# Optimization experiments

Measured on AMD Instinct MI355X. Metric: run time of the kernel, lower is better.

The kernel has to match this reference:

```python
import jax, jax.numpy as jnp
import numpy as np

N_EMBD = 1024
N_HEAD = 16
B, L = 4, 2048


def setup_inputs() -> dict:
    key = jax.random.key(0)
    ks = jax.random.split(key, 5)
    scale = 1.0 / np.sqrt(N_EMBD)
    x = jax.random.normal(ks[0], (B, L, N_EMBD), dtype=jnp.float32)
    # nn.Linear(n_embd, n_embd, bias=False) weights, stored torch-style (out, in)
    Wq = jax.random.uniform(ks[1], (N_EMBD, N_EMBD), jnp.float32, -scale, scale)
    Wk = jax.random.uniform(ks[2], (N_EMBD, N_EMBD), jnp.float32, -scale, scale)
    Wv = jax.random.uniform(ks[3], (N_EMBD, N_EMBD), jnp.float32, -scale, scale)
    Wp = jax.random.uniform(ks[4], (N_EMBD, N_EMBD), jnp.float32, -scale, scale)
    attn_mask = jnp.ones((B, L), dtype=jnp.int32)
    return {"x": x, "Wq": Wq, "Wk": Wk, "Wv": Wv, "Wp": Wp, "attn_mask": attn_mask}


def reference(x, Wq, Wk, Wv, Wp, attn_mask):
    Bq, Lq, C = x.shape
    hd = C // N_HEAD
    # torch Linear: y = x @ W.T
    def split_heads(y):
        return y.reshape(Bq, Lq, N_HEAD, hd).transpose(0, 2, 1, 3)  # (B,H,L,hd)
    q = split_heads(x @ Wq.T)
    k = split_heads(x @ Wk.T)
    v = split_heads(x @ Wv.T)
    att = jnp.einsum("bhqd,bhkd->bhqk", q, k) / np.sqrt(hd)  # (B,H,L,L)
    causal = jnp.tril(jnp.ones((Lq, Lq), dtype=bool))
    neg_inf = jnp.float32(-jnp.inf)
    att = jnp.where(causal[None, None, :, :], att, neg_inf)
    pad = (attn_mask != 0)[:, None, None, :]  # (B,1,1,L) key-side padding mask
    att = jnp.where(pad, att, neg_inf)
    att = jax.nn.softmax(att, axis=-1)
    y = jnp.einsum("bhqk,bhkd->bhqd", att, v)
    y = y.transpose(0, 2, 1, 3).reshape(Bq, Lq, C)
    return y @ Wp.T
```

## Files before the change

### kernel.cpp

```cpp
#include <hip/hip_runtime.h>

typedef __attribute__((ext_vector_type(8))) short short8;
typedef __attribute__((ext_vector_type(4))) float floatx4;

#define CEMB 1024
#define NHEAD 16
#define HD 64
#define BATCH 4
#define SEQ 2048

#define BARRIER() asm volatile("s_waitcnt lgkmcnt(0)\n\ts_barrier" ::: "memory")

__device__ __forceinline__ unsigned short f2bf(float f) {
    union { float f; unsigned int i; } x; x.f = f;
    unsigned int r = x.i + 0x7FFFu + ((x.i >> 16) & 1u);
    return (unsigned short)(r >> 16);
}
__device__ __forceinline__ unsigned int packbf_trunc(float a, float b) {
    union { float f; unsigned int u; } x, y; x.f = a; y.f = b;
    return (x.u >> 16) | (y.u & 0xFFFF0000u);
}

#define GLD16(gp, lp) \
    __builtin_amdgcn_global_load_lds((const __attribute__((address_space(1))) void*)(gp), \
                                     (__attribute__((address_space(3))) void*)(lp), 16, 0, 0)

__global__ void cast_x(const float* __restrict__ src, unsigned short* __restrict__ dst, int n4) {
    int i = blockIdx.x * blockDim.x + threadIdx.x;
    if (i < n4) {
        float4 v = ((const float4*)src)[i];
        ushort4 o;
        o.x = f2bf(v.x); o.y = f2bf(v.y); o.z = f2bf(v.z); o.w = f2bf(v.w);
        ((ushort4*)dst)[i] = o;
    }
}

__global__ void cast_w(const float* __restrict__ w0, const float* __restrict__ w1,
                       const float* __restrict__ w2, const float* __restrict__ w3,
                       unsigned short* __restrict__ o0, unsigned short* __restrict__ o1,
                       unsigned short* __restrict__ o2, unsigned short* __restrict__ o3) {
    int which = blockIdx.y;
    const float* src = which == 0 ? w0 : which == 1 ? w1 : which == 2 ? w2 : w3;
    unsigned short* dst = which == 0 ? o0 : which == 1 ? o1 : which == 2 ? o2 : o3;
    float scale = (which == 0) ? 0.125f * 1.44269504088896f : 1.0f;
    int i = blockIdx.x * blockDim.x + threadIdx.x;
    float4 v = ((const float4*)src)[i];
    ushort4 o;
    o.x = f2bf(v.x * scale); o.y = f2bf(v.y * scale);
    o.z = f2bf(v.z * scale); o.w = f2bf(v.w * scale);
    ((ushort4*)dst)[i] = o;
}


#define MFMA __builtin_amdgcn_mfma_f32_16x16x32_bf16

#define PH(Ab, Bb) do {                                                         \
    short8 af[4][2], bfr[2][2];                                                 \
    _Pragma("unroll")                                                           \
    for (int mm = 0; mm < 4; ++mm) {                                            \
        af[mm][0] = *(const short8*)((Ab) + aOffR + mm*1024 + ck0);             \
        af[mm][1] = *(const short8*)((Ab) + aOffR + mm*1024 + ck1);             \
    }                                                                           \
    _Pragma("unroll")                                                           \
    for (int nn = 0; nn < 2; ++nn) {                                            \
        bfr[nn][0] = *(const short8*)((Bb) + bOffR + nn*1024 + ck0);            \
        bfr[nn][1] = *(const short8*)((Bb) + bOffR + nn*1024 + ck1);            \
    }                                                                           \
    __builtin_amdgcn_s_setprio(1);                                              \
    _Pragma("unroll")                                                           \
    for (int mm = 0; mm < 4; ++mm)                                              \
        _Pragma("unroll")                                                       \
        for (int nn = 0; nn < 2; ++nn) {                                        \
            acc[mm][nn] = MFMA(af[mm][0], bfr[nn][0], acc[mm][nn], 0,0,0);      \
            acc[mm][nn] = MFMA(af[mm][1], bfr[nn][1], acc[mm][nn], 0,0,0);      \
        }                                                                       \
    __builtin_amdgcn_s_setprio(0);                                              \
    __builtin_amdgcn_sched_barrier(0);                                          \
} while (0)

#define STAGE(Ab, Bb, k0) do {                                                  \
    GLD16(aS + (k0),             (Ab) + aLS);                                   \
    GLD16(aS + (k0) +  8 * CEMB, (Ab) + aLS + 512);                             \
    GLD16(aS + (k0) + 16 * CEMB, (Ab) + aLS + 1024);                            \
    GLD16(aS + (k0) + 24 * CEMB, (Ab) + aLS + 1536);                            \
    GLD16(bS + (k0),             (Bb) + aLS);                                   \
    GLD16(bS + (k0) +  8 * CEMB, (Bb) + aLS + 512);                             \
    GLD16(bS + (k0) + 16 * CEMB, (Bb) + aLS + 1024);                            \
    GLD16(bS + (k0) + 24 * CEMB, (Bb) + aLS + 1536);                            \
} while (0)

#define PH4(Ab, Bb, t, do_stage) do {                                           \
    short8 af[4][2], bfr[2][2];                                                 \
    _Pragma("unroll")                                                           \
    for (int mm = 0; mm < 4; ++mm) {                                            \
        af[mm][0] = *(const short8*)((Ab) + aOffR + mm*1024 + ck0);             \
        af[mm][1] = *(const short8*)((Ab) + aOffR + mm*1024 + ck1);             \
    }                                                                           \
    _Pragma("unroll")                                                           \
    for (int nn = 0; nn < 2; ++nn) {                                            \
        bfr[nn][0] = *(const short8*)((Bb) + bOffR + (2+nn)*1024 + ck0);        \
        bfr[nn][1] = *(const short8*)((Bb) + bOffR + (2+nn)*1024 + ck1);        \
    }                                                                           \
    asm volatile("s_waitcnt lgkmcnt(0)\n\ts_barrier" ::: "memory");             \
    __builtin_amdgcn_sched_barrier(0);                                          \
    if (do_stage) STAGE(Ab, Bb, ((t) + 2) * 64);                                \
    __builtin_amdgcn_s_setprio(1);                                              \
    _Pragma("unroll")                                                           \
    for (int mm = 0; mm < 4; ++mm)                                              \
        _Pragma("unroll")                                                       \
        for (int nn = 0; nn < 2; ++nn) {                                        \
            acc[mm][2+nn] = MFMA(af[mm][0], bfr[nn][0], acc[mm][2+nn], 0,0,0);  \
            acc[mm][2+nn] = MFMA(af[mm][1], bfr[nn][1], acc[mm][2+nn], 0,0,0);  \
        }                                                                       \
    __builtin_amdgcn_s_setprio(0);                                              \
    __builtin_amdgcn_sched_barrier(0);                                          \
} while (0)

#define TILE(t, drain, do_stage) do {                                           \
    unsigned short* Ab = &As[(t) & 1][0];                                       \
    unsigned short* Bb = &Bs[(t) & 1][0];                                       \
    if (drain) { asm volatile("s_waitcnt vmcnt(0)" ::: "memory"); }             \
    else       { asm volatile("s_waitcnt vmcnt(8)" ::: "memory"); }             \
    asm volatile("s_barrier" ::: "memory");                                     \
    PH(Ab, Bb);                                                                 \
    PH4(Ab, Bb, t, do_stage);                                                   \
} while (0)

__launch_bounds__(256, 2)
__global__ void gemm_128(const unsigned short* __restrict__ A,
                         const unsigned short* __restrict__ W,
                         void* __restrict__ O0, void* __restrict__ O1,
                         void* __restrict__ O2, int mode, int ntn) {
    __shared__ unsigned short As[2][8192];
    __shared__ unsigned short Bs[2][8192];

    int nwg = gridDim.x;
    int bid = blockIdx.x;
    int wg = (bid & 7) * (nwg >> 3) + (bid >> 3);
    int cpr = ntn >> 2;
    int c = wg >> 5, r = wg & 31;
    int cm = c / cpr, cn = c - cm * cpr;
    int mt = cm * 8 + (r >> 2);
    int nt = cn * 4 + (r & 3);
    int m0 = mt * 128, n0 = nt * 128;

    int tid = threadIdx.x;
    int wave = tid >> 6, lane = tid & 63;
    int l16 = lane & 15, quad = lane >> 4;
    int wm = wave >> 1, wn = wave & 1;

    int srow = lane >> 3;
    int scol = ((lane & 7) ^ srow) * 8;
    const unsigned short* aS = A + (size_t)(m0 + wave * 32 + srow) * CEMB + scol;
    const unsigned short* bS = W + (size_t)(n0 + wave * 32 + srow) * CEMB + scol;
    int aLS = wave * 2048;

    int aOffR = (wm * 64 + l16) * 64;
    int bOffR = (wn * 64 + l16) * 64;
    int ck0 = (quad ^ (l16 & 7)) * 8;
    int ck1 = ck0 ^ 32;

    floatx4 acc[4][4];
    #pragma unroll
    for (int mm = 0; mm < 4; ++mm)
        #pragma unroll
        for (int nn = 0; nn < 4; ++nn) acc[mm][nn] = (floatx4){0.f, 0.f, 0.f, 0.f};

    STAGE(&As[0][0], &Bs[0][0], 0);
    STAGE(&As[1][0], &Bs[1][0], 64);

    #pragma unroll 2
    for (int t = 0; t < 14; ++t) { TILE(t, false, true); }
    TILE(14, false, false);
    TILE(15, true, false);

    if (mode == 1) {
        float* Of = (float*)O0;
        #pragma unroll
        for (int mf = 0; mf < 4; ++mf)
            #pragma unroll
            for (int j = 0; j < 4; ++j) {
                int m = m0 + wm * 64 + mf * 16 + quad * 4 + j;
                #pragma unroll
                for (int nf = 0; nf < 4; ++nf) {
                    int n = n0 + wn * 64 + nf * 16 + l16;
                    Of[(size_t)m * CEMB + n] = acc[mf][nf][j];
                }
            }
    } else {
        int which = n0 >> 10;
        unsigned short* out = (unsigned short*)(which == 0 ? O0 : which == 1 ? O1 : O2);
        if (which < 2) {
            #pragma unroll
            for (int mf = 0; mf < 4; ++mf)
                #pragma unroll
                for (int j = 0; j < 4; ++j) {
                    int m = m0 + wm * 64 + mf * 16 + quad * 4 + j;
                    int bb = m >> 11, ll = m & (SEQ - 1);
                    #pragma unroll
                    for (int nf = 0; nf < 4; ++nf) {
                        int n = (n0 & (CEMB - 1)) + wn * 64 + nf * 16 + l16;
                        int h = n >> 6, d = n & (HD - 1);
                        out[(size_t)((bb * NHEAD + h) * SEQ + ll) * HD + d] =
                            f2bf(acc[mf][nf][j]);
                    }
                }
        } else {
            #pragma unroll
            for (int mf = 0; mf < 4; ++mf) {
                int m = m0 + wm * 64 + mf * 16 + quad * 4;
                int bb = m >> 11, ll = m & (SEQ - 1);
                #pragma unroll
                for (int nf = 0; nf < 4; ++nf) {
                    int n = (n0 & (CEMB - 1)) + wn * 64 + nf * 16 + l16;
                    int h = n >> 6, d = n & (HD - 1);
                    ushort4 o4;
                    o4.x = f2bf(acc[mf][nf][0]); o4.y = f2bf(acc[mf][nf][1]);
                    o4.z = f2bf(acc[mf][nf][2]); o4.w = f2bf(acc[mf][nf][3]);
                    *(ushort4*)&out[(size_t)((bb * NHEAD + h) * HD + d) * SEQ + ll] = o4;
                }
            }
        }
    }
}

__launch_bounds__(256, 2)
__global__ void attn_mfma(const unsigned short* __restrict__ Qb,
                          const unsigned short* __restrict__ Kb,
                          const unsigned short* __restrict__ Vtg,
                          const int* __restrict__ amask,
                          unsigned short* __restrict__ Yb) {
    __shared__ unsigned short Ks[64 * 64];
    __shared__ unsigned short Vs[64 * 64];
    __shared__ unsigned short Ps[128 * 64];

    int tid = threadIdx.x;
    int wave = tid >> 6;
    int lane = tid & 63;
    int l16 = lane & 15;
    int quad = lane >> 4;
    int l7 = l16 & 7;

    int n = blockIdx.x;
    int rr = n >> 8;
    int i = n & 255;
    int base = i & 15;
    int bh = (i >> 4) + (rr << 4);
    int qt = (rr == 0) ? base
           : (rr == 1) ? 15 - base
           : (rr == 2) ? (base ^ 8)
                       : 15 - (base ^ 8);

    int bidx = bh >> 4;
    int h = bh & (NHEAD - 1);
    size_t hbase = (size_t)bh * SEQ * HD;

    int r0 = tid >> 3, p0 = tid & 7;
    int cl = p0 ^ (r0 & 7);
    unsigned short* kDst0 = Ks + r0 * 64 + p0 * 8;
    unsigned short* kDst1 = kDst0 + 32 * 64;
    unsigned short* vDst0 = Vs + r0 * 64 + p0 * 8;
    unsigned short* vDst1 = vDst0 + 32 * 64;
    const unsigned short* kSrc0 = Kb + hbase + (size_t)r0 * HD + cl * 8;
    const unsigned short* kSrc1 = kSrc0 + (size_t)32 * HD;
    const unsigned short* vSrc0 = Vtg + hbase + (size_t)r0 * SEQ + cl * 8;
    const unsigned short* vSrc1 = vSrc0 + (size_t)32 * SEQ;
    const int* mSrc = amask + bidx * SEQ + quad * 4;

    int q0 = qt * 128;
    int nkt = 2 * qt + 2;

    short8 qf[2][2];
    #pragma unroll
    for (int qsub = 0; qsub < 2; ++qsub)
        #pragma unroll
        for (int kk = 0; kk < 2; ++kk)
            qf[qsub][kk] = *(const short8*)(Qb + hbase +
                (size_t)(q0 + wave * 32 + qsub * 16 + l16) * HD + kk * 32 + quad * 8);

    short8 kr0 = *(const short8*)(kSrc0);
    short8 kr1 = *(const short8*)(kSrc1);
    short8 vr0 = *(const short8*)(vSrc0);
    short8 vr1 = *(const short8*)(vSrc1);
    int4 cmi[4];
    #pragma unroll
    for (int t = 0; t < 4; ++t) cmi[t] = *(const int4*)(mSrc + t * 16);

    floatx4 o[2][4];
    #pragma unroll
    for (int qsub = 0; qsub < 2; ++qsub)
        #pragma unroll
        for (int t = 0; t < 4; ++t) o[qsub][t] = (floatx4){0.f, 0.f, 0.f, 0.f};
    float ls[2] = {0.f, 0.f};

    int qw = q0 + wave * 32;

    for (int jt = 0; jt < nkt; ++jt) {
        BARRIER();
        *(short8*)kDst0 = kr0;
        *(short8*)kDst1 = kr1;
        *(short8*)vDst0 = vr0;
        *(short8*)vDst1 = vr1;
        int4 cm[4];
        #pragma unroll
        for (int t = 0; t < 4; ++t) cm[t] = cmi[t];
        if (jt + 1 < nkt) {
            size_t ko = (size_t)(jt + 1) * 64;
            kr0 = *(const short8*)(kSrc0 + ko * HD);
            kr1 = *(const short8*)(kSrc1 + ko * HD);
            vr0 = *(const short8*)(vSrc0 + ko);
            vr1 = *(const short8*)(vSrc1 + ko);
            #pragma unroll
            for (int t = 0; t < 4; ++t) cmi[t] = *(const int4*)(mSrc + (jt + 1) * 64 + t * 16);
        }
        BARRIER();

        if (jt * 64 <= qw + 31) {
            floatx4 sc[2][4];
            #pragma unroll
            for (int qsub = 0; qsub < 2; ++qsub)
                #pragma unroll
                for (int t = 0; t < 4; ++t) sc[qsub][t] = (floatx4){0.f, 0.f, 0.f, 0.f};
            #pragma unroll
            for (int kk = 0; kk < 2; ++kk)
                #pragma unroll
                for (int t = 0; t < 4; ++t) {
                    short8 aK = *(const short8*)(Ks + (t * 16 + l16) * 64 +
                                                 ((kk * 4 + quad) ^ l7) * 8);
                    #pragma unroll
                    for (int qsub = 0; qsub < 2; ++qsub)
                        sc[qsub][t] = __builtin_amdgcn_mfma_f32_16x16x32_bf16(
                            aK, qf[qsub][kk], sc[qsub][t], 0, 0, 0);
                }

            bool needc = (jt * 64 + 63 > qw);

            #pragma unroll
            for (int qsub = 0; qsub < 2; ++qsub) {
                int qi = q0 + wave * 32 + qsub * 16 + l16;
                #pragma unroll
                for (int t = 0; t < 4; ++t) {
                    int kb = jt * 64 + t * 16 + quad * 4;
                    float p[4];
                    #pragma unroll
                    for (int j = 0; j < 4; ++j) {
                        float sv = sc[qsub][t][j];
                        if (needc) sv = (kb + j <= qi) ? sv : -1e30f;
                        sv = cm[t][j] ? sv : -1e30f;
                        p[j] = __builtin_amdgcn_exp2f(sv);
                        ls[qsub] += p[j];
                    }
                    int row = wave * 32 + qsub * 16 + l16;
                    int pos = (t * 2 + (quad >> 1)) ^ l7;
                    uint2 pk;
                    pk.x = packbf_trunc(p[0], p[1]);
                    pk.y = packbf_trunc(p[2], p[3]);
                    *(uint2*)(Ps + row * 64 + pos * 8 + (quad & 1) * 4) = pk;
                }
            }

            #pragma unroll
            for (int kk = 0; kk < 2; ++kk) {
                short8 pa[2];
                #pragma unroll
                for (int qsub = 0; qsub < 2; ++qsub)
                    pa[qsub] = *(const short8*)(Ps + (wave * 32 + qsub * 16 + l16) * 64 +
                                                ((kk * 4 + quad) ^ l7) * 8);
                #pragma unroll
                for (int t = 0; t < 4; ++t) {
                    short8 vb = *(const short8*)(Vs + (t * 16 + l16) * 64 +
                                                 ((kk * 4 + quad) ^ l7) * 8);
                    #pragma unroll
                    for (int qsub = 0; qsub < 2; ++qsub)
                        o[qsub][t] = __builtin_amdgcn_mfma_f32_16x16x32_bf16(
                            pa[qsub], vb, o[qsub][t], 0, 0, 0);
                }
            }
        }
    }

    #pragma unroll
    for (int qsub = 0; qsub < 2; ++qsub) {
        ls[qsub] += __shfl_xor(ls[qsub], 16, 64);
        ls[qsub] += __shfl_xor(ls[qsub], 32, 64);
    }

    #pragma unroll
    for (int qsub = 0; qsub < 2; ++qsub)
        #pragma unroll
        for (int j = 0; j < 4; ++j) {
            float lq = __shfl(ls[qsub], quad * 4 + j, 64);
            float inv = 1.0f / lq;
            size_t row = (size_t)bidx * SEQ + q0 + wave * 32 + qsub * 16 + quad * 4 + j;
            #pragma unroll
            for (int t = 0; t < 4; ++t)
                Yb[row * CEMB + h * HD + t * 16 + l16] = f2bf(o[qsub][t][j] * inv);
        }
}

extern "C" void kernel_launch(void* const* d_in, const int* in_sizes, int n_in,
                              void* d_out, int out_size, void* d_ws, size_t ws_size,
                              hipStream_t stream) {
    const float* x  = (const float*)d_in[0];
    const float* Wq = (const float*)d_in[1];
    const float* Wk = (const float*)d_in[2];
    const float* Wv = (const float*)d_in[3];
    const float* Wp = (const float*)d_in[4];
    const int* amask = (const int*)d_in[5];

    char* ws = (char*)d_ws;
    unsigned short* xb  = (unsigned short*)(ws + 0);
    unsigned short* Wqb = (unsigned short*)(ws + (16u << 20));
    unsigned short* Wkb = (unsigned short*)(ws + (18u << 20));
    unsigned short* Wvb = (unsigned short*)(ws + (20u << 20));
    unsigned short* Wpb = (unsigned short*)(ws + (22u << 20));
    unsigned short* Qb  = (unsigned short*)(ws + (24u << 20));
    unsigned short* Kb  = (unsigned short*)(ws + (40u << 20));
    unsigned short* Vtg = (unsigned short*)(ws + (56u << 20));
    unsigned short* Yb  = (unsigned short*)(ws + (72u << 20));

    const int NX4 = (BATCH * SEQ * CEMB) / 4;
    const int NW4 = (CEMB * CEMB) / 4;
    cast_x<<<dim3(NX4 / 256), 256, 0, stream>>>(x, xb, NX4);
    cast_w<<<dim3(NW4 / 256, 4), 256, 0, stream>>>(Wq, Wk, Wv, Wp, Wqb, Wkb, Wvb, Wpb);

    gemm_128<<<dim3(1536), 256, 0, stream>>>(
        xb, Wqb, (void*)Qb, (void*)Kb, (void*)Vtg, 0, 24);

    attn_mfma<<<dim3(1024), 256, 0, stream>>>(Qb, Kb, Vtg, amask, Yb);

    gemm_128<<<dim3(512), 256, 0, stream>>>(
        Yb, Wpb, d_out, nullptr, nullptr, 1, 8);
}
```

Measured before the change: 247.3 us.

## Halve GEMM K-tile to 32 for higher occupancy; add setprio around attention MFMAs

The projection GEMM now stages 32-wide K tiles instead of 64, which halves shared memory per block and doubles the number of pipeline iterations. The launch bound moves from 2 to 4 blocks per CU, and the LDS swizzle and staging addresses are rewritten for the narrower tile. The goal is more resident waves to hide memory latency, at the cost of more barriers per unit of work and less work per sync. Separately, the attention kernel's QK and PV MFMA loops are wrapped in s_setprio to favour matrix issue.

```diff
diff --git a/kernel.cpp b/kernel.cpp
--- a/kernel.cpp
+++ b/kernel.cpp
@@ -54,85 +54,57 @@
 
 #define MFMA __builtin_amdgcn_mfma_f32_16x16x32_bf16
 
-#define PH(Ab, Bb) do {                                                         \
-    short8 af[4][2], bfr[2][2];                                                 \
+#define STAGE(Ab, Bb, k0) do {                                                  \
+    GLD16(aS + (k0),             (Ab) + aLS);                                   \
+    GLD16(aS + (k0) + 64 * CEMB, (Ab) + aLS + 2048);                            \
+    GLD16(bS + (k0),             (Bb) + aLS);                                   \
+    GLD16(bS + (k0) + 64 * CEMB, (Bb) + aLS + 2048);                            \
+} while (0)
+
+#define TILE(t, drain, do_stage) do {                                           \
+    unsigned short* Ab = &As[(t) & 1][0];                                       \
+    unsigned short* Bb = &Bs[(t) & 1][0];                                       \
+    if (drain) { asm volatile("s_waitcnt vmcnt(0)" ::: "memory"); }             \
+    else       { asm volatile("s_waitcnt vmcnt(4)" ::: "memory"); }             \
+    asm volatile("s_barrier" ::: "memory");                                     \
+    short8 af[4], bfr[4];                                                       \
     _Pragma("unroll")                                                           \
-    for (int mm = 0; mm < 4; ++mm) {                                            \
-        af[mm][0] = *(const short8*)((Ab) + aOffR + mm*1024 + ck0);             \
-        af[mm][1] = *(const short8*)((Ab) + aOffR + mm*1024 + ck1);             \
-    }                                                                           \
+    for (int mm = 0; mm < 4; ++mm)                                              \
+        af[mm] = *(const short8*)((Ab) + aOffR + mm * 512 + ck);                \
     _Pragma("unroll")                                                           \
-    for (int nn = 0; nn < 2; ++nn) {                                            \
-        bfr[nn][0] = *(const short8*)((Bb) + bOffR + nn*1024 + ck0);            \
-        bfr[nn][1] = *(const short8*)((Bb) + bOffR + nn*1024 + ck1);            \
-    }                                                                           \
+    for (int nn = 0; nn < 2; ++nn)                                              \
+        bfr[nn] = *(const short8*)((Bb) + bOffR + nn * 512 + ck);               \
     __builtin_amdgcn_s_setprio(1);                                              \
     _Pragma("unroll")                                                           \
     for (int mm = 0; mm < 4; ++mm)                                              \
         _Pragma("unroll")                                                       \
-        for (int nn = 0; nn < 2; ++nn) {                                        \
-            acc[mm][nn] = MFMA(af[mm][0], bfr[nn][0], acc[mm][nn], 0,0,0);      \
-            acc[mm][nn] = MFMA(af[mm][1], bfr[nn][1], acc[mm][nn], 0,0,0);      \
-        }                                                                       \
+        for (int nn = 0; nn < 2; ++nn)                                          \
+            acc[mm][nn] = MFMA(af[mm], bfr[nn], acc[mm][nn], 0, 0, 0);          \
     __builtin_amdgcn_s_setprio(0);                                              \
     __builtin_amdgcn_sched_barrier(0);                                          \
-} while (0)
-
-#define STAGE(Ab, Bb, k0) do {                                                  \
-    GLD16(aS + (k0),             (Ab) + aLS);                                   \
-    GLD16(aS + (k0) +  8 * CEMB, (Ab) + aLS + 512);                             \
-    GLD16(aS + (k0) + 16 * CEMB, (Ab) + aLS + 1024);                            \
-    GLD16(aS + (k0) + 24 * CEMB, (Ab) + aLS + 1536);                            \
-    GLD16(bS + (k0),             (Bb) + aLS);                                   \
-    GLD16(bS + (k0) +  8 * CEMB, (Bb) + aLS + 512);                             \
-    GLD16(bS + (k0) + 16 * CEMB, (Bb) + aLS + 1024);                            \
-    GLD16(bS + (k0) + 24 * CEMB, (Bb) + aLS + 1536);                            \
-} while (0)
-
-#define PH4(Ab, Bb, t, do_stage) do {                                           \
-    short8 af[4][2], bfr[2][2];                                                 \
     _Pragma("unroll")                                                           \
-    for (int mm = 0; mm < 4; ++mm) {                                            \
-        af[mm][0] = *(const short8*)((Ab) + aOffR + mm*1024 + ck0);             \
-        af[mm][1] = *(const short8*)((Ab) + aOffR + mm*1024 + ck1);             \
-    }                                                                           \
-    _Pragma("unroll")                                                           \
-    for (int nn = 0; nn < 2; ++nn) {                                            \
-        bfr[nn][0] = *(const short8*)((Bb) + bOffR + (2+nn)*1024 + ck0);        \
-        bfr[nn][1] = *(const short8*)((Bb) + bOffR + (2+nn)*1024 + ck1);        \
-    }                                                                           \
+    for (int nn = 2; nn < 4; ++nn)                                              \
+        bfr[nn] = *(const short8*)((Bb) + bOffR + nn * 512 + ck);               \
     asm volatile("s_waitcnt lgkmcnt(0)\n\ts_barrier" ::: "memory");             \
     __builtin_amdgcn_sched_barrier(0);                                          \
-    if (do_stage) STAGE(Ab, Bb, ((t) + 2) * 64);                                \
+    if (do_stage) STAGE(Ab, Bb, ((t) + 2) * 32);                                \
     __builtin_amdgcn_s_setprio(1);                                              \
     _Pragma("unroll")                                                           \
     for (int mm = 0; mm < 4; ++mm)                                              \
         _Pragma("unroll")                                                       \
-        for (int nn = 0; nn < 2; ++nn) {                                        \
-            acc[mm][2+nn] = MFMA(af[mm][0], bfr[nn][0], acc[mm][2+nn], 0,0,0);  \
-            acc[mm][2+nn] = MFMA(af[mm][1], bfr[nn][1], acc[mm][2+nn], 0,0,0);  \
-        }                                                                       \
+        for (int nn = 2; nn < 4; ++nn)                                          \
+            acc[mm][nn] = MFMA(af[mm], bfr[nn], acc[mm][nn], 0, 0, 0);          \
     __builtin_amdgcn_s_setprio(0);                                              \
     __builtin_amdgcn_sched_barrier(0);                                          \
 } while (0)
 
-#define TILE(t, drain, do_stage) do {                                           \
-    unsigned short* Ab = &As[(t) & 1][0];                                       \
-    unsigned short* Bb = &Bs[(t) & 1][0];                                       \
-    if (drain) { asm volatile("s_waitcnt vmcnt(0)" ::: "memory"); }             \
-    else       { asm volatile("s_waitcnt vmcnt(8)" ::: "memory"); }             \
-    asm volatile("s_barrier" ::: "memory");                                     \
-    PH(Ab, Bb);                                                                 \
-    PH4(Ab, Bb, t, do_stage);                                                   \
-} while (0)
-
-__launch_bounds__(256, 2)
+__launch_bounds__(256, 4)
 __global__ void gemm_128(const unsigned short* __restrict__ A,
                          const unsigned short* __restrict__ W,
                          void* __restrict__ O0, void* __restrict__ O1,
                          void* __restrict__ O2, int mode, int ntn) {
-    __shared__ unsigned short As[2][8192];
-    __shared__ unsigned short Bs[2][8192];
+    __shared__ unsigned short As[2][4096];
+    __shared__ unsigned short Bs[2][4096];
 
     int nwg = gridDim.x;
     int bid = blockIdx.x;
@@ -149,16 +121,16 @@
     int l16 = lane & 15, quad = lane >> 4;
     int wm = wave >> 1, wn = wave & 1;
 
-    int srow = lane >> 3;
-    int scol = ((lane & 7) ^ srow) * 8;
-    const unsigned short* aS = A + (size_t)(m0 + wave * 32 + srow) * CEMB + scol;
-    const unsigned short* bS = W + (size_t)(n0 + wave * 32 + srow) * CEMB + scol;
-    int aLS = wave * 2048;
-
-    int aOffR = (wm * 64 + l16) * 64;
-    int bOffR = (wn * 64 + l16) * 64;
-    int ck0 = (quad ^ (l16 & 7)) * 8;
-    int ck1 = ck0 ^ 32;
+    int r0 = tid >> 2;
+    int p0 = tid & 3;
+    int cl = (p0 ^ (r0 & 3)) * 8;
+    const unsigned short* aS = A + (size_t)(m0 + r0) * CEMB + cl;
+    const unsigned short* bS = W + (size_t)(n0 + r0) * CEMB + cl;
+    int aLS = wave * 512;
+
+    int aOffR = (wm * 64 + l16) * 32;
+    int bOffR = (wn * 64 + l16) * 32;
+    int ck = (quad ^ (l16 & 3)) * 8;
 
     floatx4 acc[4][4];
     #pragma unroll
@@ -167,12 +139,12 @@
         for (int nn = 0; nn < 4; ++nn) acc[mm][nn] = (floatx4){0.f, 0.f, 0.f, 0.f};
 
     STAGE(&As[0][0], &Bs[0][0], 0);
-    STAGE(&As[1][0], &Bs[1][0], 64);
+    STAGE(&As[1][0], &Bs[1][0], 32);
 
     #pragma unroll 2
-    for (int t = 0; t < 14; ++t) { TILE(t, false, true); }
-    TILE(14, false, false);
-    TILE(15, true, false);
+    for (int t = 0; t < 30; ++t) { TILE(t, false, true); }
+    TILE(30, false, false);
+    TILE(31, true, false);
 
     if (mode == 1) {
         float* Of = (float*)O0;
@@ -321,6 +293,7 @@
             for (int qsub = 0; qsub < 2; ++qsub)
                 #pragma unroll
                 for (int t = 0; t < 4; ++t) sc[qsub][t] = (floatx4){0.f, 0.f, 0.f, 0.f};
+            __builtin_amdgcn_s_setprio(1);
             #pragma unroll
             for (int kk = 0; kk < 2; ++kk)
                 #pragma unroll
@@ -332,6 +305,7 @@
                         sc[qsub][t] = __builtin_amdgcn_mfma_f32_16x16x32_bf16(
                             aK, qf[qsub][kk], sc[qsub][t], 0, 0, 0);
                 }
+            __builtin_amdgcn_s_setprio(0);
 
             bool needc = (jt * 64 + 63 > qw);
 
@@ -359,6 +333,7 @@
                 }
             }
 
+            __builtin_amdgcn_s_setprio(1);
             #pragma unroll
             for (int kk = 0; kk < 2; ++kk) {
                 short8 pa[2];
@@ -376,6 +351,7 @@
                             pa[qsub], vb, o[qsub][t], 0, 0, 0);
                 }
             }
+            __builtin_amdgcn_s_setprio(0);
         }
     }
 
```

Result: slower. 294.8 us (+19.2%).
